# Performance work log

Hardware: AMD Instinct MI355X
Metric: run time of the kernel (lower is better)

Reference implementation:

```python
import jax, jax.numpy as jnp
import numpy as np

HEADS = 4
DIM_HEAD = 32
LN_EPS = 1e-5


def setup_inputs() -> dict:
    key = jax.random.key(0)
    ks = jax.random.split(key, 3)
    B, C, H, W = 16, 128, 128, 128
    hidden = HEADS * DIM_HEAD  # 128
    x = jax.random.normal(ks[0], (B, C, H, W), dtype=jnp.float32)
    w_qkv = jax.random.normal(ks[1], (3 * hidden, C), dtype=jnp.float32) * (1.0 / np.sqrt(C))
    w_out = jax.random.normal(ks[2], (C, hidden), dtype=jnp.float32) * (1.0 / np.sqrt(hidden))
    b_out = jnp.zeros((C,), dtype=jnp.float32)
    ln_g = jnp.ones((C,), dtype=jnp.float32)
    ln_b = jnp.zeros((C,), dtype=jnp.float32)
    return {"x": x, "w_qkv": w_qkv, "w_out": w_out, "b_out": b_out, "ln_g": ln_g, "ln_b": ln_b}


def reference(x, w_qkv, w_out, b_out, ln_g, ln_b):
    B, C, H, W = x.shape
    n = H * W
    scale = DIM_HEAD ** -0.5
    # 1x1 conv == channel matmul: [B, 3*hidden, H, W]
    qkv = jnp.einsum('bcxy,oc->boxy', x, w_qkv)
    # chunk(3, dim=1) then rearrange 'b (h c) x y -> b h c (x y)'
    qkv = qkv.reshape(B, 3, HEADS, DIM_HEAD, n)
    q, k, v = qkv[:, 0], qkv[:, 1], qkv[:, 2]  # each [B, h, d, n]
    q = jax.nn.softmax(q, axis=-2) * scale      # softmax over feature dim d
    k = jax.nn.softmax(k, axis=-1)              # softmax over token dim n
    # linear attention: context [B,h,d,e], then out [B,h,e,n]
    context = jnp.einsum('bhdn,bhen->bhde', k, v)
    out = jnp.einsum('bhde,bhdn->bhen', context, q)
    out = out.reshape(B, HEADS * DIM_HEAD, H, W)
    # to_out: 1x1 conv with bias, then channel LayerNorm (biased variance)
    out = jnp.einsum('bcxy,oc->boxy', out, w_out) + b_out[None, :, None, None]
    mean = jnp.mean(out, axis=1, keepdims=True)
    var = jnp.var(out, axis=1, keepdims=True)
    return (out - mean) / jnp.sqrt(var + LN_EPS) * ln_g[None, :, None, None] + ln_b[None, :, None, None]
```

## Files before the change

kernel.cpp:

```cpp
#include <hip/hip_runtime.h>

typedef unsigned short ushort_t;
typedef __attribute__((ext_vector_type(8))) short bf16x8;
typedef __attribute__((ext_vector_type(4))) float f32x4;

#define NPOS 16384
#define CIN 128
#define O3  384
#define HID 128
#define GA  64
#define TA  4

__device__ inline float b2f(ushort_t u) {
    union { unsigned int i; float f; } z; z.i = ((unsigned int)u) << 16; return z.f;
}
__device__ inline ushort_t f2b(float f) {
    union { float f; unsigned int u; } x; x.f = f;
    unsigned int lsb = (x.u >> 16) & 1u;
    unsigned int r = x.u + 0x7fffu + lsb;
    return (ushort_t)(r >> 16);
}

__global__ __launch_bounds__(256) void k_cvt(const float* __restrict__ wq,
                                             ushort_t* __restrict__ wq_bf) {
    int i = blockIdx.x * 256 + threadIdx.x;
    wq_bf[i] = f2b(wq[i]);
}

__device__ inline void stage_x64(const float* __restrict__ x, int t, ushort_t (*xt)[136]) {
    int q4 = t & 15;
    int ch0 = t >> 4;
    const float* xp = x + q4 * 4;
#pragma unroll
    for (int it = 0; it < 8; ++it) {
        int c = it * 16 + ch0;
        float4 v = *(const float4*)(xp + (size_t)c * NPOS);
        xt[q4 * 4 + 0][c] = f2b(v.x);
        xt[q4 * 4 + 1][c] = f2b(v.y);
        xt[q4 * 4 + 2][c] = f2b(v.z);
        xt[q4 * 4 + 3][c] = f2b(v.w);
    }
}


__global__ __launch_bounds__(256) void k_ctxsum2(const float* __restrict__ x,
                                                 const ushort_t* __restrict__ wq,
                                                 float* __restrict__ kexp_part,
                                                 float* __restrict__ ctx_part,
                                                 ushort_t* __restrict__ qt) {
    __shared__ __align__(16) ushort_t xt[64][136];
    __shared__ ushort_t kb[4][32][40];
    __shared__ ushort_t vb[4][32][40];
    int t = threadIdx.x, b = blockIdx.y, bx = blockIdx.x;
    int w = t >> 6, l = t & 63, lr = l & 15, lq = l >> 4;

    bf16x8 qa[2][4], ka[2][4], va[2][4];
#pragma unroll
    for (int g = 0; g < 2; ++g)
#pragma unroll
        for (int kk = 0; kk < 4; ++kk) {
            qa[g][kk] = *(const bf16x8*)(wq + (size_t)(      w * 32 + g * 16 + lr) * CIN + kk * 32 + lq * 8);
            ka[g][kk] = *(const bf16x8*)(wq + (size_t)(128 + w * 32 + g * 16 + lr) * CIN + kk * 32 + lq * 8);
            va[g][kk] = *(const bf16x8*)(wq + (size_t)(256 + w * 32 + g * 16 + lr) * CIN + kk * 32 + lq * 8);
        }

    f32x4 cacc[2][2];
#pragma unroll
    for (int mt = 0; mt < 2; ++mt)
#pragma unroll
        for (int nt = 0; nt < 2; ++nt) cacc[mt][nt] = (f32x4){0.f, 0.f, 0.f, 0.f};
    float sacc[2][4];
#pragma unroll
    for (int g = 0; g < 2; ++g)
#pragma unroll
        for (int r = 0; r < 4; ++r) sacc[g][r] = 0.f;

    const float scale = 0.17677669529663687f;

    for (int tt = 0; tt < TA; ++tt) {
        int tile = bx * TA + tt;
        stage_x64(x + (size_t)b * CIN * NPOS + tile * 64, t, xt);
        __syncthreads();

        ushort4 qpk[2][2][2];

#pragma unroll
        for (int c4 = 0; c4 < 2; ++c4) {
            bf16x8 xb[2][4];
#pragma unroll
            for (int nt = 0; nt < 2; ++nt)
#pragma unroll
                for (int kk = 0; kk < 4; ++kk)
                    xb[nt][kk] = *(const bf16x8*)(&xt[c4 * 32 + nt * 16 + lr][kk * 32 + lq * 8]);

            f32x4 kacc[2][2], vacc[2][2], qacc[2][2];
#pragma unroll
            for (int g = 0; g < 2; ++g)
#pragma unroll
                for (int nt = 0; nt < 2; ++nt) {
                    kacc[g][nt] = (f32x4){0.f, 0.f, 0.f, 0.f};
                    vacc[g][nt] = (f32x4){0.f, 0.f, 0.f, 0.f};
                    qacc[g][nt] = (f32x4){0.f, 0.f, 0.f, 0.f};
                }
#pragma unroll
            for (int g = 0; g < 2; ++g)
#pragma unroll
                for (int nt = 0; nt < 2; ++nt)
#pragma unroll
                    for (int kk = 0; kk < 4; ++kk) {
                        kacc[g][nt] = __builtin_amdgcn_mfma_f32_16x16x32_bf16(ka[g][kk], xb[nt][kk], kacc[g][nt], 0, 0, 0);
                        vacc[g][nt] = __builtin_amdgcn_mfma_f32_16x16x32_bf16(va[g][kk], xb[nt][kk], vacc[g][nt], 0, 0, 0);
                        qacc[g][nt] = __builtin_amdgcn_mfma_f32_16x16x32_bf16(qa[g][kk], xb[nt][kk], qacc[g][nt], 0, 0, 0);
                    }

#pragma unroll
            for (int g = 0; g < 2; ++g)
#pragma unroll
                for (int nt = 0; nt < 2; ++nt)
#pragma unroll
                    for (int r = 0; r < 4; ++r) {
                        float e_ = __expf(kacc[g][nt][r]);
                        sacc[g][r] += e_;
                        kb[w][g * 16 + lq * 4 + r][nt * 16 + lr] = f2b(e_);
                        vb[w][g * 16 + lq * 4 + r][nt * 16 + lr] = f2b(vacc[g][nt][r]);
                    }

            bf16x8 ak[2], av[2];
#pragma unroll
            for (int mt = 0; mt < 2; ++mt) ak[mt] = *(const bf16x8*)(&kb[w][mt * 16 + lr][lq * 8]);
#pragma unroll
            for (int nt = 0; nt < 2; ++nt) av[nt] = *(const bf16x8*)(&vb[w][nt * 16 + lr][lq * 8]);
#pragma unroll
            for (int mt = 0; mt < 2; ++mt)
#pragma unroll
                for (int nt = 0; nt < 2; ++nt)
                    cacc[mt][nt] = __builtin_amdgcn_mfma_f32_16x16x32_bf16(ak[mt], av[nt], cacc[mt][nt], 0, 0, 0);

#pragma unroll
            for (int nt = 0; nt < 2; ++nt) {
                float m = -1e30f;
#pragma unroll
                for (int g = 0; g < 2; ++g)
#pragma unroll
                    for (int r = 0; r < 4; ++r) m = fmaxf(m, qacc[g][nt][r]);
                m = fmaxf(m, __shfl_xor(m, 16));
                m = fmaxf(m, __shfl_xor(m, 32));
                float ee[2][4], s = 0.f;
#pragma unroll
                for (int g = 0; g < 2; ++g)
#pragma unroll
                    for (int r = 0; r < 4; ++r) { ee[g][r] = __expf(qacc[g][nt][r] - m); s += ee[g][r]; }
                s += __shfl_xor(s, 16);
                s += __shfl_xor(s, 32);
                float inv = scale / s;
#pragma unroll
                for (int g = 0; g < 2; ++g) {
                    ushort4 u;
                    u.x = f2b(ee[g][0] * inv); u.y = f2b(ee[g][1] * inv);
                    u.z = f2b(ee[g][2] * inv); u.w = f2b(ee[g][3] * inv);
                    qpk[c4][nt][g] = u;
                }
            }
        }

        __syncthreads();

        {
            ushort_t* qlds = (ushort_t*)&xt[0][0];
#pragma unroll
            for (int c4 = 0; c4 < 2; ++c4)
#pragma unroll
                for (int nt = 0; nt < 2; ++nt)
#pragma unroll
                    for (int g = 0; g < 2; ++g) {
                        int pos = c4 * 32 + nt * 16 + lr;
                        int byteoff = pos * 256 + (((w * 32 + g * 16 + lq * 4) * 2) ^ ((pos & 7) << 4));
                        *(ushort4*)((char*)qlds + byteoff) = qpk[c4][nt][g];
                    }
        }
        __syncthreads();

        {
            const uint4* s4 = (const uint4*)&xt[0][0];
            uint4* d4 = (uint4*)(qt + ((size_t)b * 256 + tile) * 8192);
#pragma unroll
            for (int it = 0; it < 4; ++it) d4[it * 256 + t] = s4[it * 256 + t];
        }
        __syncthreads();
    }

#pragma unroll
    for (int mt = 0; mt < 2; ++mt)
#pragma unroll
        for (int nt = 0; nt < 2; ++nt)
#pragma unroll
            for (int r = 0; r < 4; ++r)
                ctx_part[(((size_t)bx * 16 + b) * 4 + w) * 1024 +
                         (size_t)(mt * 16 + lq * 4 + r) * 32 + nt * 16 + lr] = cacc[mt][nt][r];

#pragma unroll
    for (int g = 0; g < 2; ++g)
#pragma unroll
        for (int r = 0; r < 4; ++r) {
            float s = sacc[g][r];
            s += __shfl_xor(s, 1); s += __shfl_xor(s, 2);
            s += __shfl_xor(s, 4); s += __shfl_xor(s, 8);
            if (lr == 0)
                kexp_part[((size_t)bx * 16 + b) * 128 + w * 32 + g * 16 + lq * 4 + r] = s;
        }
}

__global__ __launch_bounds__(256) void k_weff2(const float* __restrict__ wo,
                                               const float* __restrict__ ctx_part,
                                               const float* __restrict__ kexp_part,
                                               ushort_t* __restrict__ weff) {
    int bh = blockIdx.x, b = bh >> 2, h = bh & 3;
    __shared__ float wos[128][32];
    __shared__ float cs[32][33];
    __shared__ float kinv[32];
    int t = threadIdx.x;

    float4 a = {0.f, 0.f, 0.f, 0.f};
#pragma unroll 16
    for (int g = 0; g < GA; ++g) {
        float4 v = *(const float4*)&ctx_part[(((size_t)g * 16 + b) * 4 + h) * 1024 + t * 4];
        a.x += v.x; a.y += v.y; a.z += v.z; a.w += v.w;
    }
    {
        int d = t >> 3, e0 = (t & 7) * 4;
        cs[d][e0 + 0] = a.x; cs[d][e0 + 1] = a.y; cs[d][e0 + 2] = a.z; cs[d][e0 + 3] = a.w;
    }
    if (t < 32) {
        float s = 0.f;
#pragma unroll 16
        for (int g = 0; g < GA; ++g) s += kexp_part[((size_t)g * 16 + b) * 128 + h * 32 + t];
        kinv[t] = 1.0f / s;
    }
#pragma unroll
    for (int k = 0; k < 16; ++k) {
        int idx = k * 256 + t; int c = idx >> 5, e = idx & 31;
        wos[c][e] = wo[(size_t)c * HID + h * 32 + e];
    }
    __syncthreads();
#pragma unroll
    for (int k = 0; k < 16; ++k) {
        int idx = k * 256 + t; int c = idx >> 5, d = idx & 31;
        float s = 0.f;
#pragma unroll
        for (int e = 0; e < 32; ++e) s += wos[c][e] * cs[d][e];
        weff[((size_t)b * HID + c) * HID + h * 32 + d] = f2b(s * kinv[d]);
    }
}

__global__ __launch_bounds__(256) void k_outf2(const ushort_t* __restrict__ qt,
                                               const ushort_t* __restrict__ weff,
                                               const float* __restrict__ bout,
                                               const float* __restrict__ lng,
                                               const float* __restrict__ lnb,
                                               float* __restrict__ out) {
    __shared__ float redS[4][64], redQ[4][64];
    int t = threadIdx.x, b = blockIdx.y, tile = blockIdx.x, p0 = tile * 64;
    int w = t >> 6, l = t & 63, lr = l & 15, lq = l >> 4;

    const char* qbase = (const char*)(qt + ((size_t)b * 256 + tile) * 8192);

    bf16x8 wa[2][4];
#pragma unroll
    for (int g = 0; g < 2; ++g)
#pragma unroll
        for (int kk = 0; kk < 4; ++kk)
            wa[g][kk] = *(const bf16x8*)(weff + ((size_t)b * HID + w * 32 + g * 16 + lr) * HID + kk * 32 + lq * 8);

    f32x4 oacc[2][4];
#pragma unroll
    for (int g = 0; g < 2; ++g)
#pragma unroll
        for (int j = 0; j < 4; ++j) oacc[g][j] = (f32x4){0.f, 0.f, 0.f, 0.f};
#pragma unroll
    for (int j = 0; j < 4; ++j) {
        bf16x8 sb[4];
#pragma unroll
        for (int kk = 0; kk < 4; ++kk) {
            int pos = j * 16 + lr;
            sb[kk] = *(const bf16x8*)(qbase + pos * 256 + ((kk * 64 + lq * 16) ^ ((pos & 7) << 4)));
        }
#pragma unroll
        for (int g = 0; g < 2; ++g)
#pragma unroll
            for (int kk = 0; kk < 4; ++kk)
                oacc[g][j] = __builtin_amdgcn_mfma_f32_16x16x32_bf16(wa[g][kk], sb[kk], oacc[g][j], 0, 0, 0);
    }

    float bias_[2][4];
    float colS[4] = {0.f, 0.f, 0.f, 0.f}, colQ[4] = {0.f, 0.f, 0.f, 0.f};
#pragma unroll
    for (int g = 0; g < 2; ++g)
#pragma unroll
        for (int r = 0; r < 4; ++r) {
            int c = w * 32 + g * 16 + lq * 4 + r;
            bias_[g][r] = bout[c];
#pragma unroll
            for (int j = 0; j < 4; ++j) {
                float v = oacc[g][j][r] + bias_[g][r];
                colS[j] += v;
                colQ[j] += v * v;
            }
        }
#pragma unroll
    for (int j = 0; j < 4; ++j) {
        colS[j] += __shfl_xor(colS[j], 16); colQ[j] += __shfl_xor(colQ[j], 16);
        colS[j] += __shfl_xor(colS[j], 32); colQ[j] += __shfl_xor(colQ[j], 32);
        if (lq == 0) { redS[w][j * 16 + lr] = colS[j]; redQ[w][j * 16 + lr] = colQ[j]; }
    }
    __syncthreads();

    float mean[4], rstd[4];
#pragma unroll
    for (int j = 0; j < 4; ++j) {
        int col = j * 16 + lr;
        float S = redS[0][col] + redS[1][col] + redS[2][col] + redS[3][col];
        float Q = redQ[0][col] + redQ[1][col] + redQ[2][col] + redQ[3][col];
        float mu = S * (1.f / 128.f);
        float var = Q * (1.f / 128.f) - mu * mu;
        mean[j] = mu;
        rstd[j] = rsqrtf(var + 1e-5f);
    }

#pragma unroll
    for (int g = 0; g < 2; ++g)
#pragma unroll
        for (int r = 0; r < 4; ++r) {
            int c = w * 32 + g * 16 + lq * 4 + r;
            float gg = lng[c], lb = lnb[c];
#pragma unroll
            for (int j = 0; j < 4; ++j) {
                float v = oacc[g][j][r] + bias_[g][r];
                out[((size_t)b * HID + c) * NPOS + p0 + j * 16 + lr] =
                    (v - mean[j]) * rstd[j] * gg + lb;
            }
        }
}


__global__ __launch_bounds__(256) void k_ctxsum(const float* __restrict__ x,
                                                const ushort_t* __restrict__ wq,
                                                float* __restrict__ kexp,
                                                float* __restrict__ ctx) {
    __shared__ ushort_t xt[64][136];
    __shared__ ushort_t kb[4][32][40];
    __shared__ ushort_t vb[4][32][40];
    int t = threadIdx.x, b = blockIdx.y, p0 = blockIdx.x * 64;
    stage_x64(x + (size_t)b * CIN * NPOS + p0, t, xt);

    int w = t >> 6, l = t & 63, lr = l & 15, lq = l >> 4;

    bf16x8 ka[2][4], va[2][4];
#pragma unroll
    for (int g = 0; g < 2; ++g)
#pragma unroll
        for (int kk = 0; kk < 4; ++kk) {
            ka[g][kk] = *(const bf16x8*)(wq + (size_t)(128 + w * 32 + g * 16 + lr) * CIN + kk * 32 + lq * 8);
            va[g][kk] = *(const bf16x8*)(wq + (size_t)(256 + w * 32 + g * 16 + lr) * CIN + kk * 32 + lq * 8);
        }
    __syncthreads();

    f32x4 cacc[2][2];
#pragma unroll
    for (int mt = 0; mt < 2; ++mt)
#pragma unroll
        for (int nt = 0; nt < 2; ++nt) cacc[mt][nt] = (f32x4){0.f, 0.f, 0.f, 0.f};
    float sacc[2][4];
#pragma unroll
    for (int g = 0; g < 2; ++g)
#pragma unroll
        for (int r = 0; r < 4; ++r) sacc[g][r] = 0.f;

#pragma unroll
    for (int c4 = 0; c4 < 2; ++c4) {
        bf16x8 xb[2][4];
#pragma unroll
        for (int nt = 0; nt < 2; ++nt)
#pragma unroll
            for (int kk = 0; kk < 4; ++kk)
                xb[nt][kk] = *(const bf16x8*)(&xt[c4 * 32 + nt * 16 + lr][kk * 32 + lq * 8]);

        f32x4 kacc[2][2], vacc[2][2];
#pragma unroll
        for (int g = 0; g < 2; ++g)
#pragma unroll
            for (int nt = 0; nt < 2; ++nt) {
                kacc[g][nt] = (f32x4){0.f, 0.f, 0.f, 0.f};
                vacc[g][nt] = (f32x4){0.f, 0.f, 0.f, 0.f};
            }
#pragma unroll
        for (int g = 0; g < 2; ++g)
#pragma unroll
            for (int nt = 0; nt < 2; ++nt)
#pragma unroll
                for (int kk = 0; kk < 4; ++kk) {
                    kacc[g][nt] = __builtin_amdgcn_mfma_f32_16x16x32_bf16(ka[g][kk], xb[nt][kk], kacc[g][nt], 0, 0, 0);
                    vacc[g][nt] = __builtin_amdgcn_mfma_f32_16x16x32_bf16(va[g][kk], xb[nt][kk], vacc[g][nt], 0, 0, 0);
                }

#pragma unroll
        for (int g = 0; g < 2; ++g)
#pragma unroll
            for (int nt = 0; nt < 2; ++nt)
#pragma unroll
                for (int r = 0; r < 4; ++r) {
                    float e = __expf(kacc[g][nt][r]);
                    sacc[g][r] += e;
                    kb[w][g * 16 + lq * 4 + r][nt * 16 + lr] = f2b(e);
                    vb[w][g * 16 + lq * 4 + r][nt * 16 + lr] = f2b(vacc[g][nt][r]);
                }
        __syncthreads();

        bf16x8 ak[2], av[2];
#pragma unroll
        for (int mt = 0; mt < 2; ++mt) ak[mt] = *(const bf16x8*)(&kb[w][mt * 16 + lr][lq * 8]);
#pragma unroll
        for (int nt = 0; nt < 2; ++nt) av[nt] = *(const bf16x8*)(&vb[w][nt * 16 + lr][lq * 8]);
#pragma unroll
        for (int mt = 0; mt < 2; ++mt)
#pragma unroll
            for (int nt = 0; nt < 2; ++nt)
                cacc[mt][nt] = __builtin_amdgcn_mfma_f32_16x16x32_bf16(ak[mt], av[nt], cacc[mt][nt], 0, 0, 0);
        __syncthreads();
    }

#pragma unroll
    for (int mt = 0; mt < 2; ++mt)
#pragma unroll
        for (int nt = 0; nt < 2; ++nt)
#pragma unroll
            for (int r = 0; r < 4; ++r)
                atomicAdd(&ctx[((size_t)(b * 4 + w) * 32 + mt * 16 + lq * 4 + r) * 32 + nt * 16 + lr],
                          cacc[mt][nt][r]);

#pragma unroll
    for (int g = 0; g < 2; ++g)
#pragma unroll
        for (int r = 0; r < 4; ++r) {
            float s = sacc[g][r];
            s += __shfl_xor(s, 1); s += __shfl_xor(s, 2);
            s += __shfl_xor(s, 4); s += __shfl_xor(s, 8);
            if (lr == 0)
                atomicAdd(&kexp[(b * 4 + w) * 32 + g * 16 + lq * 4 + r], s);
        }
}

__global__ __launch_bounds__(256) void k_weff(const float* __restrict__ wo,
                                              const float* __restrict__ ctx,
                                              const float* __restrict__ kexp,
                                              ushort_t* __restrict__ weff) {
    int bh = blockIdx.x, b = bh >> 2, h = bh & 3;
    __shared__ float wos[128][32];
    __shared__ float cs[32][33];
    int t = threadIdx.x;
#pragma unroll
    for (int k = 0; k < 16; ++k) {
        int idx = k * 256 + t; int c = idx >> 5, e = idx & 31;
        wos[c][e] = wo[(size_t)c * HID + h * 32 + e];
    }
#pragma unroll
    for (int k = 0; k < 4; ++k) {
        int idx = k * 256 + t; int d = idx >> 5, e = idx & 31;
        cs[d][e] = ctx[((size_t)bh * 32 + d) * 32 + e];
    }
    __syncthreads();
#pragma unroll
    for (int k = 0; k < 16; ++k) {
        int idx = k * 256 + t; int c = idx >> 5, d = idx & 31;
        float s = 0.f;
#pragma unroll
        for (int e = 0; e < 32; ++e) s += wos[c][e] * cs[d][e];
        float kin = 1.0f / kexp[bh * 32 + d];
        weff[((size_t)b * HID + c) * HID + h * 32 + d] = f2b(s * kin);
    }
}

__global__ __launch_bounds__(256) void k_outf(const float* __restrict__ x,
                                              const ushort_t* __restrict__ wq,
                                              const ushort_t* __restrict__ weff,
                                              const float* __restrict__ bout,
                                              const float* __restrict__ lng,
                                              const float* __restrict__ lnb,
                                              float* __restrict__ out) {
    __shared__ ushort_t buf[64][136];
    __shared__ float redS[4][64], redQ[4][64];
    int t = threadIdx.x, b = blockIdx.y, p0 = blockIdx.x * 64;
    stage_x64(x + (size_t)b * CIN * NPOS + p0, t, buf);

    int w = t >> 6, l = t & 63, lr = l & 15, lq = l >> 4;

    bf16x8 qa[2][4];
#pragma unroll
    for (int g = 0; g < 2; ++g)
#pragma unroll
        for (int kk = 0; kk < 4; ++kk)
            qa[g][kk] = *(const bf16x8*)(wq + (size_t)(w * 32 + g * 16 + lr) * CIN + kk * 32 + lq * 8);
    __syncthreads();

    f32x4 qacc[2][4];
#pragma unroll
    for (int g = 0; g < 2; ++g)
#pragma unroll
        for (int j = 0; j < 4; ++j) qacc[g][j] = (f32x4){0.f, 0.f, 0.f, 0.f};
#pragma unroll
    for (int j = 0; j < 4; ++j) {
        bf16x8 xb[4];
#pragma unroll
        for (int kk = 0; kk < 4; ++kk)
            xb[kk] = *(const bf16x8*)(&buf[j * 16 + lr][kk * 32 + lq * 8]);
#pragma unroll
        for (int g = 0; g < 2; ++g)
#pragma unroll
            for (int kk = 0; kk < 4; ++kk)
                qacc[g][j] = __builtin_amdgcn_mfma_f32_16x16x32_bf16(qa[g][kk], xb[kk], qacc[g][j], 0, 0, 0);
    }
    __syncthreads();

    const float scale = 0.17677669529663687f;
#pragma unroll
    for (int j = 0; j < 4; ++j) {
        float m = -1e30f;
#pragma unroll
        for (int g = 0; g < 2; ++g)
#pragma unroll
            for (int r = 0; r < 4; ++r) m = fmaxf(m, qacc[g][j][r]);
        m = fmaxf(m, __shfl_xor(m, 16));
        m = fmaxf(m, __shfl_xor(m, 32));
        float e[2][4], s = 0.f;
#pragma unroll
        for (int g = 0; g < 2; ++g)
#pragma unroll
            for (int r = 0; r < 4; ++r) { e[g][r] = __expf(qacc[g][j][r] - m); s += e[g][r]; }
        s += __shfl_xor(s, 16);
        s += __shfl_xor(s, 32);
        float inv = scale / s;
#pragma unroll
        for (int g = 0; g < 2; ++g) {
            ushort4 u;
            u.x = f2b(e[g][0] * inv); u.y = f2b(e[g][1] * inv);
            u.z = f2b(e[g][2] * inv); u.w = f2b(e[g][3] * inv);
            *(ushort4*)(&buf[j * 16 + lr][w * 32 + g * 16 + lq * 4]) = u;
        }
    }
    __syncthreads();

    bf16x8 wa[2][4];
#pragma unroll
    for (int g = 0; g < 2; ++g)
#pragma unroll
        for (int kk = 0; kk < 4; ++kk)
            wa[g][kk] = *(const bf16x8*)(weff + ((size_t)b * HID + w * 32 + g * 16 + lr) * HID + kk * 32 + lq * 8);
    f32x4 oacc[2][4];
#pragma unroll
    for (int g = 0; g < 2; ++g)
#pragma unroll
        for (int j = 0; j < 4; ++j) oacc[g][j] = (f32x4){0.f, 0.f, 0.f, 0.f};
#pragma unroll
    for (int j = 0; j < 4; ++j) {
        bf16x8 sb[4];
#pragma unroll
        for (int kk = 0; kk < 4; ++kk)
            sb[kk] = *(const bf16x8*)(&buf[j * 16 + lr][kk * 32 + lq * 8]);
#pragma unroll
        for (int g = 0; g < 2; ++g)
#pragma unroll
            for (int kk = 0; kk < 4; ++kk)
                oacc[g][j] = __builtin_amdgcn_mfma_f32_16x16x32_bf16(wa[g][kk], sb[kk], oacc[g][j], 0, 0, 0);
    }

    float vals[2][4][4];
    float colS[4] = {0.f, 0.f, 0.f, 0.f}, colQ[4] = {0.f, 0.f, 0.f, 0.f};
#pragma unroll
    for (int g = 0; g < 2; ++g)
#pragma unroll
        for (int r = 0; r < 4; ++r) {
            int c = w * 32 + g * 16 + lq * 4 + r;
            float bias = bout[c];
#pragma unroll
            for (int j = 0; j < 4; ++j) {
                float v = oacc[g][j][r] + bias;
                vals[g][j][r] = v;
                colS[j] += v;
                colQ[j] += v * v;
            }
        }
#pragma unroll
    for (int j = 0; j < 4; ++j) {
        colS[j] += __shfl_xor(colS[j], 16); colQ[j] += __shfl_xor(colQ[j], 16);
        colS[j] += __shfl_xor(colS[j], 32); colQ[j] += __shfl_xor(colQ[j], 32);
        if (lq == 0) { redS[w][j * 16 + lr] = colS[j]; redQ[w][j * 16 + lr] = colQ[j]; }
    }
    __syncthreads();

    float mean[4], rstd[4];
#pragma unroll
    for (int j = 0; j < 4; ++j) {
        int col = j * 16 + lr;
        float S = redS[0][col] + redS[1][col] + redS[2][col] + redS[3][col];
        float Q = redQ[0][col] + redQ[1][col] + redQ[2][col] + redQ[3][col];
        float mu = S * (1.f / 128.f);
        float var = Q * (1.f / 128.f) - mu * mu;
        mean[j] = mu;
        rstd[j] = rsqrtf(var + 1e-5f);
    }

#pragma unroll
    for (int g = 0; g < 2; ++g)
#pragma unroll
        for (int r = 0; r < 4; ++r) {
            int c = w * 32 + g * 16 + lq * 4 + r;
            float gg = lng[c], lb = lnb[c];
#pragma unroll
            for (int j = 0; j < 4; ++j)
                out[((size_t)b * HID + c) * NPOS + p0 + j * 16 + lr] =
                    (vals[g][j][r] - mean[j]) * rstd[j] * gg + lb;
        }
}

extern "C" void kernel_launch(void* const* d_in, const int* in_sizes, int n_in,
                              void* d_out, int out_size, void* d_ws, size_t ws_size,
                              hipStream_t stream) {
    const float* x    = (const float*)d_in[0];
    const float* wqkv = (const float*)d_in[1];
    const float* wout = (const float*)d_in[2];
    const float* bout = (const float*)d_in[3];
    const float* lng  = (const float*)d_in[4];
    const float* lnb  = (const float*)d_in[5];
    float* out = (float*)d_out;

    char* ws = (char*)d_ws;

    const size_t off_kexp = 0;
    const size_t off_ctxp = 524288;
    const size_t off_wqbf = 17301504;
    const size_t off_weff = 17399808;
    const size_t off_qt   = 17924096;
    const size_t NEED     = 85032960;

    if (ws_size >= NEED) {
        float*    kexp_part = (float*)(ws + off_kexp);
        float*    ctx_part  = (float*)(ws + off_ctxp);
        ushort_t* wq_bf     = (ushort_t*)(ws + off_wqbf);
        ushort_t* weff      = (ushort_t*)(ws + off_weff);
        ushort_t* qt        = (ushort_t*)(ws + off_qt);

        k_cvt<<<dim3(192), dim3(256), 0, stream>>>(wqkv, wq_bf);
        k_ctxsum2<<<dim3(GA, 16), dim3(256), 0, stream>>>(x, wq_bf, kexp_part, ctx_part, qt);
        k_weff2<<<dim3(64), dim3(256), 0, stream>>>(wout, ctx_part, kexp_part, weff);
        k_outf2<<<dim3(NPOS / 64, 16), dim3(256), 0, stream>>>(qt, weff, bout, lng, lnb, out);
    } else {
        float*    kexp  = (float*)ws;
        float*    ctx   = (float*)(ws + 8192);
        ushort_t* wq_bf = (ushort_t*)(ws + 270336);
        ushort_t* weff  = (ushort_t*)(ws + 368640);

        hipMemsetAsync(ws, 0, 270336, stream);

        k_cvt<<<dim3(192), dim3(256), 0, stream>>>(wqkv, wq_bf);
        k_ctxsum<<<dim3(NPOS / 64, 16), dim3(256), 0, stream>>>(x, wq_bf, kexp, ctx);
        k_weff<<<dim3(64), dim3(256), 0, stream>>>(wout, ctx, kexp, weff);
        k_outf<<<dim3(NPOS / 64, 16), dim3(256), 0, stream>>>(x, wq_bf, weff, bout, lng, lnb, out);
    }
}
```

Measured before the change: 334.9 us.

## Split x bf16 transpose into prep kernel; compute q softmax in output kernel

Adds a k_prep kernel that converts x to bf16 once and writes swizzled position-major tiles to global memory. The context kernel then reads these compact tiles with register prefetch instead of restaging fp32 x. The q projection and its feature softmax move out of the context kernel into the output kernel, which recomputes q from the bf16 x tile. This shortens the context pass and its 64-block grid, at the cost of one extra launch and a second full read of the bf16 x buffer.

Result: no change. 335.9 us (+0.3%).

```diff
diff --git a/kernel.cpp b/kernel.cpp
--- a/kernel.cpp
+++ b/kernel.cpp
@@ -43,23 +43,40 @@
 }
 
 
-__global__ __launch_bounds__(256) void k_ctxsum2(const float* __restrict__ x,
+__global__ __launch_bounds__(256) void k_prep(const float* __restrict__ x,
+                                              ushort_t* __restrict__ xtg) {
+    __shared__ __align__(16) ushort_t xt[64][136];
+    int t = threadIdx.x, tile = blockIdx.x, b = blockIdx.y;
+    stage_x64(x + (size_t)b * CIN * NPOS + tile * 64, t, xt);
+    __syncthreads();
+    int w = t >> 6, l = t & 63;
+    char* gbase = (char*)(xtg + ((size_t)b * 256 + tile) * 8192);
+#pragma unroll
+    for (int i = 0; i < 4; ++i) {
+        int off = (w * 4 + i) * 1024 + l * 16;
+        int pos = off >> 8;
+        int d0  = off & 255;
+        int s   = (pos & 7) << 4;
+        uint4 v = *(const uint4*)((const char*)&xt[0][0] + pos * 272 + (d0 ^ s));
+        *(uint4*)(gbase + off) = v;
+    }
+}
+
+__global__ __launch_bounds__(256) void k_ctxsum3(const ushort_t* __restrict__ xtg,
                                                  const ushort_t* __restrict__ wq,
                                                  float* __restrict__ kexp_part,
-                                                 float* __restrict__ ctx_part,
-                                                 ushort_t* __restrict__ qt) {
-    __shared__ __align__(16) ushort_t xt[64][136];
+                                                 float* __restrict__ ctx_part) {
+    __shared__ __align__(16) ushort_t xs[8192];
     __shared__ ushort_t kb[4][32][40];
     __shared__ ushort_t vb[4][32][40];
     int t = threadIdx.x, b = blockIdx.y, bx = blockIdx.x;
     int w = t >> 6, l = t & 63, lr = l & 15, lq = l >> 4;
 
-    bf16x8 qa[2][4], ka[2][4], va[2][4];
+    bf16x8 ka[2][4], va[2][4];
 #pragma unroll
     for (int g = 0; g < 2; ++g)
 #pragma unroll
         for (int kk = 0; kk < 4; ++kk) {
-            qa[g][kk] = *(const bf16x8*)(wq + (size_t)(      w * 32 + g * 16 + lr) * CIN + kk * 32 + lq * 8);
             ka[g][kk] = *(const bf16x8*)(wq + (size_t)(128 + w * 32 + g * 16 + lr) * CIN + kk * 32 + lq * 8);
             va[g][kk] = *(const bf16x8*)(wq + (size_t)(256 + w * 32 + g * 16 + lr) * CIN + kk * 32 + lq * 8);
         }
@@ -75,14 +92,21 @@
 #pragma unroll
         for (int r = 0; r < 4; ++r) sacc[g][r] = 0.f;
 
-    const float scale = 0.17677669529663687f;
+    const char* gtile0 = (const char*)(xtg + ((size_t)b * 256 + bx * TA) * 8192);
+
+    uint4 rg[4];
+#pragma unroll
+    for (int i = 0; i < 4; ++i) rg[i] = *(const uint4*)(gtile0 + (i * 256 + t) * 16);
 
     for (int tt = 0; tt < TA; ++tt) {
-        int tile = bx * TA + tt;
-        stage_x64(x + (size_t)b * CIN * NPOS + tile * 64, t, xt);
+#pragma unroll
+        for (int i = 0; i < 4; ++i) *((uint4*)xs + i * 256 + t) = rg[i];
+        if (tt + 1 < TA) {
+            const char* gt = gtile0 + (tt + 1) * 16384;
+#pragma unroll
+            for (int i = 0; i < 4; ++i) rg[i] = *(const uint4*)(gt + (i * 256 + t) * 16);
+        }
         __syncthreads();
-
-        ushort4 qpk[2][2][2];
 
 #pragma unroll
         for (int c4 = 0; c4 < 2; ++c4) {
@@ -90,17 +114,19 @@
 #pragma unroll
             for (int nt = 0; nt < 2; ++nt)
 #pragma unroll
-                for (int kk = 0; kk < 4; ++kk)
-                    xb[nt][kk] = *(const bf16x8*)(&xt[c4 * 32 + nt * 16 + lr][kk * 32 + lq * 8]);
-
-            f32x4 kacc[2][2], vacc[2][2], qacc[2][2];
+                for (int kk = 0; kk < 4; ++kk) {
+                    int pos = c4 * 32 + nt * 16 + lr;
+                    xb[nt][kk] = *(const bf16x8*)((const char*)xs + pos * 256 +
+                                                  ((kk * 64 + lq * 16) ^ ((pos & 7) << 4)));
+                }
+
+            f32x4 kacc[2][2], vacc[2][2];
 #pragma unroll
             for (int g = 0; g < 2; ++g)
 #pragma unroll
                 for (int nt = 0; nt < 2; ++nt) {
                     kacc[g][nt] = (f32x4){0.f, 0.f, 0.f, 0.f};
                     vacc[g][nt] = (f32x4){0.f, 0.f, 0.f, 0.f};
-                    qacc[g][nt] = (f32x4){0.f, 0.f, 0.f, 0.f};
                 }
 #pragma unroll
             for (int g = 0; g < 2; ++g)
@@ -110,7 +136,6 @@
                     for (int kk = 0; kk < 4; ++kk) {
                         kacc[g][nt] = __builtin_amdgcn_mfma_f32_16x16x32_bf16(ka[g][kk], xb[nt][kk], kacc[g][nt], 0, 0, 0);
                         vacc[g][nt] = __builtin_amdgcn_mfma_f32_16x16x32_bf16(va[g][kk], xb[nt][kk], vacc[g][nt], 0, 0, 0);
-                        qacc[g][nt] = __builtin_amdgcn_mfma_f32_16x16x32_bf16(qa[g][kk], xb[nt][kk], qacc[g][nt], 0, 0, 0);
                     }
 
 #pragma unroll
@@ -135,56 +160,6 @@
 #pragma unroll
                 for (int nt = 0; nt < 2; ++nt)
                     cacc[mt][nt] = __builtin_amdgcn_mfma_f32_16x16x32_bf16(ak[mt], av[nt], cacc[mt][nt], 0, 0, 0);
-
-#pragma unroll
-            for (int nt = 0; nt < 2; ++nt) {
-                float m = -1e30f;
-#pragma unroll
-                for (int g = 0; g < 2; ++g)
-#pragma unroll
-                    for (int r = 0; r < 4; ++r) m = fmaxf(m, qacc[g][nt][r]);
-                m = fmaxf(m, __shfl_xor(m, 16));
-                m = fmaxf(m, __shfl_xor(m, 32));
-                float ee[2][4], s = 0.f;
-#pragma unroll
-                for (int g = 0; g < 2; ++g)
-#pragma unroll
-                    for (int r = 0; r < 4; ++r) { ee[g][r] = __expf(qacc[g][nt][r] - m); s += ee[g][r]; }
-                s += __shfl_xor(s, 16);
-                s += __shfl_xor(s, 32);
-                float inv = scale / s;
-#pragma unroll
-                for (int g = 0; g < 2; ++g) {
-                    ushort4 u;
-                    u.x = f2b(ee[g][0] * inv); u.y = f2b(ee[g][1] * inv);
-                    u.z = f2b(ee[g][2] * inv); u.w = f2b(ee[g][3] * inv);
-                    qpk[c4][nt][g] = u;
-                }
-            }
-        }
-
-        __syncthreads();
-
-        {
-            ushort_t* qlds = (ushort_t*)&xt[0][0];
-#pragma unroll
-            for (int c4 = 0; c4 < 2; ++c4)
-#pragma unroll
-                for (int nt = 0; nt < 2; ++nt)
-#pragma unroll
-                    for (int g = 0; g < 2; ++g) {
-                        int pos = c4 * 32 + nt * 16 + lr;
-                        int byteoff = pos * 256 + (((w * 32 + g * 16 + lq * 4) * 2) ^ ((pos & 7) << 4));
-                        *(ushort4*)((char*)qlds + byteoff) = qpk[c4][nt][g];
-                    }
-        }
-        __syncthreads();
-
-        {
-            const uint4* s4 = (const uint4*)&xt[0][0];
-            uint4* d4 = (uint4*)(qt + ((size_t)b * 256 + tile) * 8192);
-#pragma unroll
-            for (int it = 0; it < 4; ++it) d4[it * 256 + t] = s4[it * 256 + t];
         }
         __syncthreads();
     }
@@ -252,17 +227,85 @@
     }
 }
 
-__global__ __launch_bounds__(256) void k_outf2(const ushort_t* __restrict__ qt,
+__global__ __launch_bounds__(256) void k_outf3(const ushort_t* __restrict__ xtg,
+                                               const ushort_t* __restrict__ wq,
                                                const ushort_t* __restrict__ weff,
                                                const float* __restrict__ bout,
                                                const float* __restrict__ lng,
                                                const float* __restrict__ lnb,
                                                float* __restrict__ out) {
+    __shared__ __align__(16) ushort_t xs[8192];
     __shared__ float redS[4][64], redQ[4][64];
     int t = threadIdx.x, b = blockIdx.y, tile = blockIdx.x, p0 = tile * 64;
     int w = t >> 6, l = t & 63, lr = l & 15, lq = l >> 4;
 
-    const char* qbase = (const char*)(qt + ((size_t)b * 256 + tile) * 8192);
+    const char* gt = (const char*)(xtg + ((size_t)b * 256 + tile) * 8192);
+    uint4 rg[4];
+#pragma unroll
+    for (int i = 0; i < 4; ++i) rg[i] = *(const uint4*)(gt + (i * 256 + t) * 16);
+
+    bf16x8 qa[2][4];
+#pragma unroll
+    for (int g = 0; g < 2; ++g)
+#pragma unroll
+        for (int kk = 0; kk < 4; ++kk)
+            qa[g][kk] = *(const bf16x8*)(wq + (size_t)(w * 32 + g * 16 + lr) * CIN + kk * 32 + lq * 8);
+
+#pragma unroll
+    for (int i = 0; i < 4; ++i) *((uint4*)xs + i * 256 + t) = rg[i];
+    __syncthreads();
+
+    f32x4 qacc[2][4];
+#pragma unroll
+    for (int g = 0; g < 2; ++g)
+#pragma unroll
+        for (int j = 0; j < 4; ++j) qacc[g][j] = (f32x4){0.f, 0.f, 0.f, 0.f};
+#pragma unroll
+    for (int j = 0; j < 4; ++j) {
+        bf16x8 xb[4];
+#pragma unroll
+        for (int kk = 0; kk < 4; ++kk) {
+            int pos = j * 16 + lr;
+            xb[kk] = *(const bf16x8*)((const char*)xs + pos * 256 +
+                                      ((kk * 64 + lq * 16) ^ ((pos & 7) << 4)));
+        }
+#pragma unroll
+        for (int g = 0; g < 2; ++g)
+#pragma unroll
+            for (int kk = 0; kk < 4; ++kk)
+                qacc[g][j] = __builtin_amdgcn_mfma_f32_16x16x32_bf16(qa[g][kk], xb[kk], qacc[g][j], 0, 0, 0);
+    }
+    __syncthreads();
+
+    const float scale = 0.17677669529663687f;
+#pragma unroll
+    for (int j = 0; j < 4; ++j) {
+        float m = -1e30f;
+#pragma unroll
+        for (int g = 0; g < 2; ++g)
+#pragma unroll
+            for (int r = 0; r < 4; ++r) m = fmaxf(m, qacc[g][j][r]);
+        m = fmaxf(m, __shfl_xor(m, 16));
+        m = fmaxf(m, __shfl_xor(m, 32));
+        float e[2][4], s = 0.f;
+#pragma unroll
+        for (int g = 0; g < 2; ++g)
+#pragma unroll
+            for (int r = 0; r < 4; ++r) { e[g][r] = __expf(qacc[g][j][r] - m); s += e[g][r]; }
+        s += __shfl_xor(s, 16);
+        s += __shfl_xor(s, 32);
+        float inv = scale / s;
+        int pos = j * 16 + lr;
+#pragma unroll
+        for (int g = 0; g < 2; ++g) {
+            ushort4 u;
+            u.x = f2b(e[g][0] * inv); u.y = f2b(e[g][1] * inv);
+            u.z = f2b(e[g][2] * inv); u.w = f2b(e[g][3] * inv);
+            int byteoff = pos * 256 + (((w * 32 + g * 16 + lq * 4) * 2) ^ ((pos & 7) << 4));
+            *(ushort4*)((char*)xs + byteoff) = u;
+        }
+    }
+    __syncthreads();
 
     bf16x8 wa[2][4];
 #pragma unroll
@@ -270,7 +313,6 @@
 #pragma unroll
         for (int kk = 0; kk < 4; ++kk)
             wa[g][kk] = *(const bf16x8*)(weff + ((size_t)b * HID + w * 32 + g * 16 + lr) * HID + kk * 32 + lq * 8);
-
     f32x4 oacc[2][4];
 #pragma unroll
     for (int g = 0; g < 2; ++g)
@@ -282,7 +324,8 @@
 #pragma unroll
         for (int kk = 0; kk < 4; ++kk) {
             int pos = j * 16 + lr;
-            sb[kk] = *(const bf16x8*)(qbase + pos * 256 + ((kk * 64 + lq * 16) ^ ((pos & 7) << 4)));
+            sb[kk] = *(const bf16x8*)((const char*)xs + pos * 256 +
+                                      ((kk * 64 + lq * 16) ^ ((pos & 7) << 4)));
         }
 #pragma unroll
         for (int g = 0; g < 2; ++g)
@@ -638,7 +681,7 @@
     const size_t off_ctxp = 524288;
     const size_t off_wqbf = 17301504;
     const size_t off_weff = 17399808;
-    const size_t off_qt   = 17924096;
+    const size_t off_xt   = 17924096;
     const size_t NEED     = 85032960;
 
     if (ws_size >= NEED) {
@@ -646,12 +689,13 @@
         float*    ctx_part  = (float*)(ws + off_ctxp);
         ushort_t* wq_bf     = (ushort_t*)(ws + off_wqbf);
         ushort_t* weff      = (ushort_t*)(ws + off_weff);
-        ushort_t* qt        = (ushort_t*)(ws + off_qt);
+        ushort_t* xtg       = (ushort_t*)(ws + off_xt);
 
         k_cvt<<<dim3(192), dim3(256), 0, stream>>>(wqkv, wq_bf);
-        k_ctxsum2<<<dim3(GA, 16), dim3(256), 0, stream>>>(x, wq_bf, kexp_part, ctx_part, qt);
+        k_prep<<<dim3(NPOS / 64, 16), dim3(256), 0, stream>>>(x, xtg);
+        k_ctxsum3<<<dim3(GA, 16), dim3(256), 0, stream>>>(xtg, wq_bf, kexp_part, ctx_part);
         k_weff2<<<dim3(64), dim3(256), 0, stream>>>(wout, ctx_part, kexp_part, weff);
-        k_outf2<<<dim3(NPOS / 64, 16), dim3(256), 0, stream>>>(qt, weff, bout, lng, lnb, out);
+        k_outf3<<<dim3(NPOS / 64, 16), dim3(256), 0, stream>>>(xtg, wq_bf, weff, bout, lng, lnb, out);
     } else {
         float*    kexp  = (float*)ws;
         float*    ctx   = (float*)(ws + 8192);
```
